# Kernel tuning notes

Measured on AMD Instinct MI355X. Metric: run time of the kernel, lower is better.

The kernel has to match this reference:

```python
import jax, jax.numpy as jnp
import numpy as np

B, L, W = 512, 1024, 256


def setup_inputs() -> dict:
    key = jax.random.key(0)
    ks = jax.random.split(key, 7)
    # spin configurations in {-1, +1}
    x = (jax.random.randint(ks[0], (B, L), 0, 2).astype(jnp.float32) * 2.0 - 1.0)
    s = 0.1  # param init scale
    w_ih = jax.random.normal(ks[1], (3 * W, 2), jnp.float32) * s
    w_hh = jax.random.normal(ks[2], (3 * W, W), jnp.float32) * s
    b_ih = jax.random.normal(ks[3], (3 * W,), jnp.float32) * s
    b_hh = jax.random.normal(ks[4], (3 * W,), jnp.float32) * s
    fc_w = jax.random.normal(ks[5], (2, W), jnp.float32) * s
    fc_b = jax.random.normal(ks[6], (2,), jnp.float32) * s
    return {"x": x, "w_ih": w_ih, "w_hh": w_hh, "b_ih": b_ih,
            "b_hh": b_hh, "fc_w": fc_w, "fc_b": fc_b}


def reference(x, w_ih, w_hh, b_ih, b_hh, fc_w, fc_b):
    b, n = x.shape
    w = w_hh.shape[1]
    mask = (1.0 + x) * 0.5                                   # [B, L]
    # input to step i is x[:, i-1]; step 0 uses x_init = 0 (embeds to [0.5, 0.5])
    xs = jnp.concatenate([jnp.zeros((b, 1), x.dtype), x[:, :-1]], axis=1)
    emb = jnp.stack([(xs + 1.0) * 0.5, 1.0 - (xs + 1.0) * 0.5], axis=-1)  # [B, L, 2]
    # precompute all input-side gate projections in one GEMM: [B, L, 3W]
    gi_all = jnp.einsum('blk,gk->blg', emb, w_ih) + b_ih

    def step(h, inp):
        gi, m = inp                                          # [B,3W], [B]
        gh = h @ w_hh.T + b_hh                               # [B,3W]
        i_r, i_z, i_n = jnp.split(gi, 3, axis=1)
        h_r, h_z, h_n = jnp.split(gh, 3, axis=1)
        r = jax.nn.sigmoid(i_r + h_r)
        z = jax.nn.sigmoid(i_z + h_z)
        ng = jnp.tanh(i_n + r * h_n)
        h_next = (1.0 - z) * ng + z * h                      # torch GRUCell update
        y = jax.nn.log_softmax(h_next @ fc_w.T + fc_b, axis=1)  # [B,2]
        lp = y[:, 0] * m + y[:, 1] * (1.0 - m)
        return h_next, lp

    gi_t = jnp.swapaxes(gi_all, 0, 1)                        # [L, B, 3W]
    m_t = mask.T                                             # [L, B]
    h0 = jnp.zeros((b, w), x.dtype)
    _, lps = jax.lax.scan(step, h0, (gi_t, m_t))             # lps: [L, B]
    return lps.sum(axis=0)                                   # [B]
```

## Files before the change

### kernel.cpp

```cpp
#include <hip/hip_runtime.h>
#include <math.h>

#define SL 1024
#define NW 256

typedef _Float16 half8 __attribute__((ext_vector_type(8)));
typedef _Float16 half2t __attribute__((ext_vector_type(2)));
typedef float f32x4 __attribute__((ext_vector_type(4)));

__device__ __forceinline__ float rcp_f(float v) { return __builtin_amdgcn_rcpf(v); }

__global__ __launch_bounds__(512, 2) void gru_mfma_kernel(
    const float* __restrict__ x, const float* __restrict__ w_ih,
    const float* __restrict__ w_hh, const float* __restrict__ b_ih,
    const float* __restrict__ b_hh, const float* __restrict__ fc_w,
    const float* __restrict__ fc_b, float* __restrict__ out)
{
    const int tid  = threadIdx.x;
    const int w    = tid >> 6;
    const int lane = tid & 63;
    const int c    = lane & 15;
    const int g    = lane >> 4;
    const int gl   = g & 1;
    const int row0 = blockIdx.x * 2;

    __shared__ float    x_lds[2][1026];
    __shared__ __align__(16) _Float16 h_lds[2][2][288];
    __shared__ float    dpart[SL][8][2];
    __shared__ float    wsum[8][2];

    for (int i = tid; i < 2 * SL; i += 512) {
        int b = i >> 10, j = i & (SL - 1);
        x_lds[b][1 + j] = (x[(size_t)(row0 + b) * SL + j] + 1.0f) * 0.5f;
    }
    if (tid < 2) x_lds[tid][0] = 0.5f;
    for (int i = tid; i < 2 * 2 * 288; i += 512)
        ((_Float16*)h_lds)[i] = (_Float16)0.0f;

    half8 Bf[6][8];
    #pragma unroll
    for (int f = 0; f < 6; ++f) {
        const int q = f >> 1, j = f & 1;
        const int urow = q * NW + (2 * w + j) * 16 + c;
        #pragma unroll
        for (int kt = 0; kt < 8; ++kt) {
            const float* p = w_hh + (size_t)urow * NW + kt * 32 + g * 8;
            float4 lo = *(const float4*)p;
            float4 hi = *(const float4*)(p + 4);
            half8 hb;
            hb[0] = (_Float16)lo.x; hb[1] = (_Float16)lo.y;
            hb[2] = (_Float16)lo.z; hb[3] = (_Float16)lo.w;
            hb[4] = (_Float16)hi.x; hb[5] = (_Float16)hi.y;
            hb[6] = (_Float16)hi.z; hb[7] = (_Float16)hi.w;
            Bf[f][kt] = hb;
        }
    }

    const int u = 32 * w + 16 * gl + c;
    half2t pkr, pkz, pkn;
    {
        float w0, w1;
        w0 = w_ih[2 * u]; w1 = w_ih[2 * u + 1];
        pkr[0] = (_Float16)(w1 + b_ih[u] + b_hh[u]);
        pkr[1] = (_Float16)(w0 - w1);
        w0 = w_ih[2 * (NW + u)]; w1 = w_ih[2 * (NW + u) + 1];
        pkz[0] = (_Float16)(w1 + b_ih[NW + u] + b_hh[NW + u]);
        pkz[1] = (_Float16)(w0 - w1);
        w0 = w_ih[2 * (2 * NW + u)]; w1 = w_ih[2 * (2 * NW + u) + 1];
        pkn[0] = (_Float16)(w1 + b_ih[2 * NW + u]);
        pkn[1] = (_Float16)(w0 - w1);
    }
    const float bhn = b_hh[2 * NW + u];
    const float wd  = fc_w[u] - fc_w[NW + u];
    const float bd  = fc_b[0] - fc_b[1];

    float h0 = 0.f, h1 = 0.f;

    __syncthreads();

    #pragma unroll 1
    for (int t = 0; t < SL; ++t) {
        const int cur = t & 1, nxt = cur ^ 1;

        f32x4 acc[6];
        #pragma unroll
        for (int f = 0; f < 6; ++f) { f32x4 z = {0.f, 0.f, 0.f, 0.f}; acc[f] = z; }

        #pragma unroll
        for (int kt = 0; kt < 8; ++kt) {
            half8 A = *(const half8*)&h_lds[cur][lane & 1][kt * 32 + g * 8];
            #pragma unroll
            for (int f = 0; f < 6; ++f)
                acc[f] = __builtin_amdgcn_mfma_f32_16x16x32_f16(A, Bf[f][kt], acc[f], 0, 0, 0);
        }

        const float m0 = x_lds[0][t];
        const float m1 = x_lds[1][t];

        const float ar0 = gl ? acc[1][0] : acc[0][0];
        const float ar1 = gl ? acc[1][1] : acc[0][1];
        const float az0 = gl ? acc[3][0] : acc[2][0];
        const float az1 = gl ? acc[3][1] : acc[2][1];
        const float an0 = gl ? acc[5][0] : acc[4][0];
        const float an1 = gl ? acc[5][1] : acc[4][1];

        const float cmr = (float)pkr[0], cdr = (float)pkr[1];
        const float cmz = (float)pkz[0], cdz = (float)pkz[1];
        const float cmn = (float)pkn[0], cdn = (float)pkn[1];

        const float vr0 = ar0 + fmaf(m0, cdr, cmr);
        const float rr0 = rcp_f(1.f + __expf(-vr0));
        const float vz0 = az0 + fmaf(m0, cdz, cmz);
        const float zz0 = rcp_f(1.f + __expf(-vz0));
        const float un0 = fmaf(rr0, an0 + bhn, fmaf(m0, cdn, cmn));
        const float ng0 = fmaf(-2.f, rcp_f(1.f + __expf(2.f * un0)), 1.f);
        const float hn0 = fmaf(zz0, h0 - ng0, ng0);
        const float vr1 = ar1 + fmaf(m1, cdr, cmr);
        const float rr1 = rcp_f(1.f + __expf(-vr1));
        const float vz1 = az1 + fmaf(m1, cdz, cmz);
        const float zz1 = rcp_f(1.f + __expf(-vz1));
        const float un1 = fmaf(rr1, an1 + bhn, fmaf(m1, cdn, cmn));
        const float ng1 = fmaf(-2.f, rcp_f(1.f + __expf(2.f * un1)), 1.f);
        const float hn1 = fmaf(zz1, h1 - ng1, ng1);
        h0 = hn0; h1 = hn1;

        if (g < 2) {
            h_lds[nxt][0][u] = (_Float16)hn0;
            h_lds[nxt][1][u] = (_Float16)hn1;
        }

        float p0 = (g < 2) ? hn0 * wd : 0.f;
        float p1 = (g < 2) ? hn1 * wd : 0.f;
        #pragma unroll
        for (int s = 1; s < 64; s <<= 1) {
            p0 += __shfl_xor(p0, s);
            p1 += __shfl_xor(p1, s);
        }
        if (lane == 0) { dpart[t][w][0] = p0; dpart[t][w][1] = p1; }

        __syncthreads();
    }

    float lpp0 = 0.f, lpp1 = 0.f;
    #pragma unroll 1
    for (int t = tid; t < SL; t += 512) {
        float d0 = bd, d1 = bd;
        #pragma unroll
        for (int q = 0; q < 8; ++q) { d0 += dpart[t][q][0]; d1 += dpart[t][q][1]; }
        const float u0 = (x_lds[0][t + 1] > 0.5f) ? -d0 : d0;
        const float u1 = (x_lds[1][t + 1] > 0.5f) ? -d1 : d1;
        lpp0 -= fmaxf(u0, 0.f) + __logf(1.f + __expf(-fabsf(u0)));
        lpp1 -= fmaxf(u1, 0.f) + __logf(1.f + __expf(-fabsf(u1)));
    }
    #pragma unroll
    for (int s = 1; s < 64; s <<= 1) {
        lpp0 += __shfl_xor(lpp0, s);
        lpp1 += __shfl_xor(lpp1, s);
    }
    if (lane == 0) { wsum[w][0] = lpp0; wsum[w][1] = lpp1; }
    __syncthreads();
    if (tid < 2) {
        float s = 0.f;
        #pragma unroll
        for (int q = 0; q < 8; ++q) s += wsum[q][tid];
        out[row0 + tid] = s;
    }
}

extern "C" void kernel_launch(void* const* d_in, const int* in_sizes, int n_in,
                              void* d_out, int out_size, void* d_ws, size_t ws_size,
                              hipStream_t stream) {
    const float* x    = (const float*)d_in[0];
    const float* w_ih = (const float*)d_in[1];
    const float* w_hh = (const float*)d_in[2];
    const float* b_ih = (const float*)d_in[3];
    const float* b_hh = (const float*)d_in[4];
    const float* fc_w = (const float*)d_in[5];
    const float* fc_b = (const float*)d_in[6];
    gru_mfma_kernel<<<256, 512, 0, stream>>>(
        x, w_ih, w_hh, b_ih, b_hh, fc_w, fc_b, (float*)d_out);
}
```

Before: 1.239 ms.

## Fold output-projection dot product into an MFMA and prefetch h fragments

Replaces the per-step 64-lane shuffle reduction for the output logit difference with an extra MFMA. The MFMA multiplies the previous step's fp16 hidden state by a B fragment holding fc_w[0]-fc_w[1], and its result is written to dpart one step late, with a final MFMA after the loop for the last step. The A fragments of h are now loaded from LDS right after the barrier, and the first MFMA per gate starts from a zero accumulator. This removes a shuffle chain from the serial critical path, but computes the logit with fp16 hidden state and fp16 fc weights, which changes precision.

Result: slower. 1.479 ms (+19.4%).

```diff
diff --git a/kernel.cpp b/kernel.cpp
--- a/kernel.cpp
+++ b/kernel.cpp
@@ -56,6 +56,15 @@
         }
     }
 
+    half8 B7 = (half8)(_Float16)0.0f;
+    if (c == 0) {
+        #pragma unroll
+        for (int e = 0; e < 8; ++e) {
+            const int k = w * 32 + g * 8 + e;
+            B7[e] = (_Float16)(fc_w[k] - fc_w[NW + k]);
+        }
+    }
+
     const int u = 32 * w + 16 * gl + c;
     half2t pkr, pkz, pkn;
     {
@@ -71,28 +80,34 @@
         pkn[1] = (_Float16)(w0 - w1);
     }
     const float bhn = b_hh[2 * NW + u];
-    const float wd  = fc_w[u] - fc_w[NW + u];
     const float bd  = fc_b[0] - fc_b[1];
 
+    const f32x4 zc = {0.f, 0.f, 0.f, 0.f};
     float h0 = 0.f, h1 = 0.f;
 
     __syncthreads();
+
+    half8 A0[8], Ah;
+    #pragma unroll
+    for (int kt = 0; kt < 8; ++kt)
+        A0[kt] = *(const half8*)&h_lds[0][lane & 1][kt * 32 + g * 8];
+    Ah = *(const half8*)&h_lds[0][lane & 1][w * 32 + g * 8];
 
     #pragma unroll 1
     for (int t = 0; t < SL; ++t) {
-        const int cur = t & 1, nxt = cur ^ 1;
+        const int nxt = (t & 1) ^ 1;
 
         f32x4 acc[6];
         #pragma unroll
-        for (int f = 0; f < 6; ++f) { f32x4 z = {0.f, 0.f, 0.f, 0.f}; acc[f] = z; }
-
-        #pragma unroll
-        for (int kt = 0; kt < 8; ++kt) {
-            half8 A = *(const half8*)&h_lds[cur][lane & 1][kt * 32 + g * 8];
+        for (int f = 0; f < 6; ++f)
+            acc[f] = __builtin_amdgcn_mfma_f32_16x16x32_f16(A0[0], Bf[f][0], zc, 0, 0, 0);
+        #pragma unroll
+        for (int kt = 1; kt < 8; ++kt) {
             #pragma unroll
             for (int f = 0; f < 6; ++f)
-                acc[f] = __builtin_amdgcn_mfma_f32_16x16x32_f16(A, Bf[f][kt], acc[f], 0, 0, 0);
-        }
+                acc[f] = __builtin_amdgcn_mfma_f32_16x16x32_f16(A0[kt], Bf[f][kt], acc[f], 0, 0, 0);
+        }
+        f32x4 acc7 = __builtin_amdgcn_mfma_f32_16x16x32_f16(Ah, B7, zc, 0, 0, 0);
 
         const float m0 = x_lds[0][t];
         const float m1 = x_lds[1][t];
@@ -128,18 +143,26 @@
             h_lds[nxt][0][u] = (_Float16)hn0;
             h_lds[nxt][1][u] = (_Float16)hn1;
         }
-
-        float p0 = (g < 2) ? hn0 * wd : 0.f;
-        float p1 = (g < 2) ? hn1 * wd : 0.f;
-        #pragma unroll
-        for (int s = 1; s < 64; s <<= 1) {
-            p0 += __shfl_xor(p0, s);
-            p1 += __shfl_xor(p1, s);
-        }
-        if (lane == 0) { dpart[t][w][0] = p0; dpart[t][w][1] = p1; }
-
+        if (lane == 0 && t != 0) {
+            dpart[t - 1][w][0] = acc7[0];
+            dpart[t - 1][w][1] = acc7[1];
+        }
         __syncthreads();
-    }
+
+        #pragma unroll
+        for (int kt = 0; kt < 8; ++kt)
+            A0[kt] = *(const half8*)&h_lds[nxt][lane & 1][kt * 32 + g * 8];
+        Ah = *(const half8*)&h_lds[nxt][lane & 1][w * 32 + g * 8];
+    }
+
+    {
+        f32x4 accE = __builtin_amdgcn_mfma_f32_16x16x32_f16(Ah, B7, zc, 0, 0, 0);
+        if (lane == 0) {
+            dpart[SL - 1][w][0] = accE[0];
+            dpart[SL - 1][w][1] = accE[1];
+        }
+    }
+    __syncthreads();
 
     float lpp0 = 0.f, lpp1 = 0.f;
     #pragma unroll 1
```
